# Kernel tuning notes

Hardware: AMD Instinct MI355X
Metric: run time of the kernel (lower is better)

The kernel has to match this reference:

```python
import jax, jax.numpy as jnp
import numpy as np

EPS = 1.0       # epsilon
SIGMA = 1.0     # sigma
MAX_ITER = 10   # max_iter (tol=1e-6 never triggers early stop in 10 iters for random data)


def setup_inputs() -> dict:
    key = jax.random.key(0)
    k1, k2, k3, k4 = jax.random.split(key, 4)
    B, L, K, D = 8, 2048, 2048, 64
    x = jax.random.normal(k1, (B, L, D), dtype=jnp.float32)
    y = jax.random.normal(k2, (B, K, D), dtype=jnp.float32)
    a = jax.random.uniform(k3, (B, L), dtype=jnp.float32) + 1e-3
    b = jax.random.uniform(k4, (B, K), dtype=jnp.float32) + 1e-3
    a = a / jnp.sum(a, axis=1, keepdims=True)
    b = b / jnp.sum(b, axis=1, keepdims=True)
    return {"x": x, "a": a, "y": y, "b": b}


def _make_kernel(u, v):
    # energy_squared, distance_type=2: K = -clamp(||u||^2 + ||v||^2 - 2 u.v, 0) / sigma^2
    outer = jnp.einsum('bld,bkd->blk', u, v)
    nu = jnp.sum(u * u, axis=2)
    nv = jnp.sum(v * v, axis=2)
    dist = jnp.maximum(nu[:, :, None] + nv[:, None, :] - 2.0 * outer, 0.0) / (SIGMA ** 2)
    return -dist


def _extrap(pot, logw, kern):
    # -eps * logsumexp((K + pot[:,None,:]) / eps + logw[:,None,:], axis=2)
    return -EPS * jax.scipy.special.logsumexp(
        (kern + pot[:, None, :]) / EPS + logw[:, None, :], axis=2)


def reference(x, a, y, b):
    sg = jax.lax.stop_gradient
    Kxx = _make_kernel(x, x)
    Kyy = _make_kernel(y, y)
    Kxy = _make_kernel(x, y)
    Kyx = _make_kernel(y, x)
    la = jnp.log(a)
    lb = jnp.log(b)

    # Sinkhorn fixed-point loop runs under no_grad in the original ('loop' surgery)
    sKxx, sKyy, sKxy, sKyx = sg(Kxx), sg(Kyy), sg(Kxy), sg(Kyx)
    sla, slb = sg(la), sg(lb)

    def body(i, state):
        pxx, pyy, pxy, pyx = state
        nxx = _extrap(pxx, sla, sKxx)  # dir 'xx', rev 'xx'
        nyy = _extrap(pyy, slb, sKyy)  # dir 'yy', rev 'yy'
        nxy = _extrap(pyx, slb, sKxy)  # dir 'xy', rev 'yx'
        nyx = _extrap(pxy, sla, sKyx)  # dir 'yx', rev 'xy'
        return ((nxx + pxx) * 0.5, (nyy + pyy) * 0.5,
                (nxy + pxy) * 0.5, (nyx + pyx) * 0.5)

    init = (jnp.zeros_like(la), jnp.zeros_like(lb),
            jnp.zeros_like(la), jnp.zeros_like(lb))
    pxx, pyy, pxy, pyx = jax.lax.fori_loop(0, MAX_ITER, body, init)
    pxx, pyy, pxy, pyx = sg(pxx), sg(pyy), sg(pxy), sg(pyx)

    # Final differentiable extrapolation (rho=None -> potential_transform is identity)
    f = _extrap(pxx, la, Kxx)   # (B, L)
    fe = _extrap(pxy, la, Kyx)  # (B, K)
    g = _extrap(pyy, lb, Kyy)   # (B, K)
    ge = _extrap(pyx, lb, Kxy)  # (B, L)

    diff_r = jnp.where(a == 0, 0.0, ge - f)
    diff_l = jnp.where(b == 0, 0.0, fe - g)
    res = jnp.sum(diff_r * a, axis=1) + jnp.sum(diff_l * b, axis=1)
    return jnp.mean(res)
```

## Files before the change

kernel.cpp:

```cpp
#include <hip/hip_runtime.h>
#include <stdint.h>

#define BATCH 8
#define NPTS  2048
#define DIM   64
#define VECN  (BATCH*NPTS)
#define KH    1024
#define CHUNK 64
#define NCHUNK (KH/CHUNK)

typedef __attribute__((ext_vector_type(8))) short bf16x8;
typedef __attribute__((ext_vector_type(4))) float f32x4;

#define IL2 1.4426950408889634f
#define LN2 0.6931471805599453f

__device__ inline float fexp2(float x) { return __builtin_amdgcn_exp2f(x); }
__device__ inline float flog2(float x) { return __builtin_amdgcn_logf(x); }

__device__ inline void gload_lds16(const void* g, void* l) {
  __builtin_amdgcn_global_load_lds(
      (const __attribute__((address_space(1))) uint32_t*)g,
      (__attribute__((address_space(3))) uint32_t*)l, 16, 0, 0);
}
__device__ inline void gload_lds4(const void* g, void* l) {
  __builtin_amdgcn_global_load_lds(
      (const __attribute__((address_space(1))) uint32_t*)g,
      (__attribute__((address_space(3))) uint32_t*)l, 4, 0, 0);
}

static constexpr size_t XB_OFF   = 0;
static constexpr size_t YB_OFF   = (size_t)VECN * DIM * 2;
static constexpr size_t NX2_OFF  = YB_OFF * 2;
static constexpr size_t NY2_OFF  = NX2_OFF + (size_t)VECN * 4;
static constexpr size_t LA2_OFF  = NY2_OFF + (size_t)VECN * 4;
static constexpr size_t LB2_OFF  = LA2_OFF + (size_t)VECN * 4;
static constexpr size_t POT_OFF  = LB2_OFF + (size_t)VECN * 4;
static constexpr size_t NW_OFF   = POT_OFF + (size_t)4 * VECN * 4;
static constexpr size_t PM_OFF   = NW_OFF + (size_t)4 * VECN * 8;
static constexpr size_t PS_OFF   = PM_OFF + (size_t)8 * VECN * 4;
static constexpr size_t FOUT_OFF = PS_OFF + (size_t)8 * VECN * 4;
static constexpr size_t R_OFF    = FOUT_OFF + (size_t)4 * VECN * 4;

__device__ inline ushort f2bf(float f) {
  uint32_t u = __float_as_uint(f);
  u += 0x7fffu + ((u >> 16) & 1u);
  return (ushort)(u >> 16);
}

__global__ void prep_convert(const float* __restrict__ x, const float* __restrict__ y,
                             ushort* __restrict__ xb, ushort* __restrict__ yb,
                             float* __restrict__ nx2, float* __restrict__ ny2) {
  int wid  = (blockIdx.x * blockDim.x + threadIdx.x) >> 6;
  int lane = threadIdx.x & 63;
  const float* src; ushort* dst; float* nrm; int row;
  if (wid < VECN) { src = x; dst = xb; nrm = nx2; row = wid; }
  else            { src = y; dst = yb; nrm = ny2; row = wid - VECN; }
  float v = src[(size_t)row * DIM + lane];
  dst[(size_t)row * DIM + lane] = f2bf(v);
  float sq = v * v;
  #pragma unroll
  for (int off = 32; off; off >>= 1) sq += __shfl_xor(sq, off);
  if (lane == 0) nrm[row] = sq * IL2;
}

__global__ void prep_vecs(const float* __restrict__ a, const float* __restrict__ b,
                          const float* __restrict__ nx2, const float* __restrict__ ny2,
                          float* __restrict__ la2, float* __restrict__ lb2,
                          float* __restrict__ pot, float2* __restrict__ nw) {
  int i = blockIdx.x * blockDim.x + threadIdx.x;
  float l2a = log2f(a[i]);
  float l2b = log2f(b[i]);
  la2[i] = l2a;
  lb2[i] = l2b;
  float nxv = nx2[i], nyv = ny2[i];
  nw[i]                     = make_float2(nxv, l2a);
  nw[(size_t)VECN + i]      = make_float2(nyv, l2b);
  nw[(size_t)2 * VECN + i]  = make_float2(nyv, l2b);
  nw[(size_t)3 * VECN + i]  = make_float2(nxv, l2a);
  #pragma unroll
  for (int j = 0; j < 4; ++j) pot[(size_t)j * VECN + i] = 0.f;
}

__global__ __launch_bounds__(256, 8)
void extrap_online(const ushort* __restrict__ xb, const ushort* __restrict__ yb,
                   const float* __restrict__ nx2, const float* __restrict__ ny2,
                   const float2* __restrict__ nw,
                   float* __restrict__ pm, float* __restrict__ ps) {
  __shared__ char vlds[2][CHUNK * 128];
  __shared__ char nwlds[2][CHUNK * 8];

  const int rb    = blockIdx.x >> 1;
  const int half  = blockIdx.x & 1;
  const int batch = blockIdx.y;
  const int z     = blockIdx.z;
  const ushort *U, *V; const float *nU2;
  switch (z) {
    case 0:  U = xb; V = xb; nU2 = nx2; break;
    case 1:  U = yb; V = yb; nU2 = ny2; break;
    case 2:  U = xb; V = yb; nU2 = nx2; break;
    default: U = yb; V = xb; nU2 = ny2; break;
  }
  const int lane = threadIdx.x & 63;
  const int w    = threadIdx.x >> 6;
  const int g    = lane >> 4;
  const int c    = lane & 15;
  const int rowbase = rb * 64 + w * 16;

  const ushort* Ub  = U + ((size_t)batch * NPTS + rowbase) * DIM;
  const char*   Vch = (const char*)(V + ((size_t)batch * NPTS + half * KH) * DIM);
  const char*   nwch = (const char*)(nw + (size_t)z * VECN + (size_t)batch * NPTS + half * KH);

  bf16x8 a0 = *(const bf16x8*)(Ub + (size_t)c * DIM + g * 8);
  bf16x8 a1 = *(const bf16x8*)(Ub + (size_t)c * DIM + 32 + g * 8);

  float nxr2[4];
  #pragma unroll
  for (int r = 0; r < 4; ++r) nxr2[r] = nU2[(size_t)batch * NPTS + rowbase + g * 4 + r];

  const size_t lane_voff = ((size_t)(lane >> 3)) * 128
                         + (size_t)((((lane & 7) ^ (lane >> 3)) << 4));

  float m[4], s[4];
  #pragma unroll
  for (int r = 0; r < 4; ++r) { m[r] = -INFINITY; s[r] = 0.f; }

  auto stage = [&](int p, int ck) {
    const char* gbase = Vch + (size_t)ck * CHUNK * 128;
    #pragma unroll
    for (int i = 0; i < 2; ++i) {
      int j = w * 2 + i;
      gload_lds16(gbase + (size_t)j * 1024 + lane_voff, &vlds[p][j * 1024]);
    }
    if (w == 0) {
      const char* gn = nwch + (size_t)ck * CHUNK * 8;
      gload_lds4(gn + lane * 4,       &nwlds[p][0]);
      gload_lds4(gn + 256 + lane * 4, &nwlds[p][256]);
    }
  };

  auto compute = [&](int p) {
    #pragma unroll
    for (int t = 0; t < 2; ++t) {
      const int rr0 = t * 32 + c;
      const int rr1 = rr0 + 16;
      const int x0 = (rr0 & 7) << 4;
      const char* pv0 = &vlds[p][rr0 * 128];
      const char* pv1 = &vlds[p][rr1 * 128];
      bf16x8 b0a = *(const bf16x8*)(pv0 + ((g * 16) ^ x0));
      bf16x8 b0b = *(const bf16x8*)(pv0 + ((64 + g * 16) ^ x0));
      bf16x8 b1a = *(const bf16x8*)(pv1 + ((g * 16) ^ x0));
      bf16x8 b1b = *(const bf16x8*)(pv1 + ((64 + g * 16) ^ x0));
      float2 nw0 = *(const float2*)&nwlds[p][rr0 * 8];
      float2 nw1 = *(const float2*)&nwlds[p][rr1 * 8];

      f32x4 acc0 = {0.f, 0.f, 0.f, 0.f}, acc1 = {0.f, 0.f, 0.f, 0.f};
      acc0 = __builtin_amdgcn_mfma_f32_16x16x32_bf16(a0, b0a, acc0, 0, 0, 0);
      acc0 = __builtin_amdgcn_mfma_f32_16x16x32_bf16(a1, b0b, acc0, 0, 0, 0);
      acc1 = __builtin_amdgcn_mfma_f32_16x16x32_bf16(a0, b1a, acc1, 0, 0, 0);
      acc1 = __builtin_amdgcn_mfma_f32_16x16x32_bf16(a1, b1b, acc1, 0, 0, 0);

      #pragma unroll
      for (int r = 0; r < 4; ++r) {
        float d0 = fmaxf(fmaf(-2.f * IL2, acc0[r], nxr2[r] + nw0.x), 0.f);
        float d1 = fmaxf(fmaf(-2.f * IL2, acc1[r], nxr2[r] + nw1.x), 0.f);
        float t0 = nw0.y - d0;
        float t1 = nw1.y - d1;
        float mn = fmaxf(m[r], fmaxf(t0, t1));
        s[r] = fmaf(s[r], fexp2(m[r] - mn), fexp2(t0 - mn) + fexp2(t1 - mn));
        m[r] = mn;
      }
    }
  };

  stage(0, 0);
  __syncthreads();
  int p = 0;
  for (int ck = 0; ck < NCHUNK; ++ck) {
    if (ck < NCHUNK - 1) stage(p ^ 1, ck + 1);
    compute(p);
    __syncthreads();
    p ^= 1;
  }

  #pragma unroll
  for (int r = 0; r < 4; ++r) {
    #pragma unroll
    for (int off = 1; off < 16; off <<= 1) {
      float mo = __shfl_xor(m[r], off);
      float so = __shfl_xor(s[r], off);
      float mn = fmaxf(m[r], mo);
      s[r] = fmaf(s[r], fexp2(m[r] - mn), so * fexp2(mo - mn));
      m[r] = mn;
    }
  }
  if (c == 0) {
    #pragma unroll
    for (int r = 0; r < 4; ++r) {
      size_t idx = (size_t)(half * 4 + z) * VECN + (size_t)batch * NPTS + rowbase + g * 4 + r;
      pm[idx] = m[r];
      ps[idx] = s[r];
    }
  }
}

__global__ __launch_bounds__(256, 8)
void extrap_fixed(const ushort* __restrict__ xb, const ushort* __restrict__ yb,
                  const float* __restrict__ nx2, const float* __restrict__ ny2,
                  const float2* __restrict__ nw, const float* __restrict__ Rarr,
                  float* __restrict__ pm, float* __restrict__ ps) {
  __shared__ char vlds[2][CHUNK * 128];
  __shared__ char nwlds[2][CHUNK * 8];

  const int rb    = blockIdx.x >> 1;
  const int half  = blockIdx.x & 1;
  const int batch = blockIdx.y;
  const int z     = blockIdx.z;
  const ushort *U, *V; const float *nU2;
  switch (z) {
    case 0:  U = xb; V = xb; nU2 = nx2; break;
    case 1:  U = yb; V = yb; nU2 = ny2; break;
    case 2:  U = xb; V = yb; nU2 = nx2; break;
    default: U = yb; V = xb; nU2 = ny2; break;
  }
  const int lane = threadIdx.x & 63;
  const int w    = threadIdx.x >> 6;
  const int g    = lane >> 4;
  const int c    = lane & 15;
  const int rowbase = rb * 64 + w * 16;

  const ushort* Ub  = U + ((size_t)batch * NPTS + rowbase) * DIM;
  const char*   Vch = (const char*)(V + ((size_t)batch * NPTS + half * KH) * DIM);
  const char*   nwch = (const char*)(nw + (size_t)z * VECN + (size_t)batch * NPTS + half * KH);

  bf16x8 a0 = *(const bf16x8*)(Ub + (size_t)c * DIM + g * 8);
  bf16x8 a1 = *(const bf16x8*)(Ub + (size_t)c * DIM + 32 + g * 8);

  float q[4], Rr[4];
  #pragma unroll
  for (int r = 0; r < 4; ++r) {
    size_t rowi = (size_t)batch * NPTS + rowbase + g * 4 + r;
    Rr[r] = Rarr[(size_t)z * VECN + rowi];
    q[r]  = -(nU2[rowi] + Rr[r]);
  }

  const size_t lane_voff = ((size_t)(lane >> 3)) * 128
                         + (size_t)((((lane & 7) ^ (lane >> 3)) << 4));

  float s[4] = {0.f, 0.f, 0.f, 0.f};

  auto stage = [&](int p, int ck) {
    const char* gbase = Vch + (size_t)ck * CHUNK * 128;
    #pragma unroll
    for (int i = 0; i < 2; ++i) {
      int j = w * 2 + i;
      gload_lds16(gbase + (size_t)j * 1024 + lane_voff, &vlds[p][j * 1024]);
    }
    if (w == 0) {
      const char* gn = nwch + (size_t)ck * CHUNK * 8;
      gload_lds4(gn + lane * 4,       &nwlds[p][0]);
      gload_lds4(gn + 256 + lane * 4, &nwlds[p][256]);
    }
  };

  auto compute = [&](int p) {
    #pragma unroll
    for (int t = 0; t < 2; ++t) {
      const int rr0 = t * 32 + c;
      const int rr1 = rr0 + 16;
      const int x0 = (rr0 & 7) << 4;
      const char* pv0 = &vlds[p][rr0 * 128];
      const char* pv1 = &vlds[p][rr1 * 128];
      bf16x8 b0a = *(const bf16x8*)(pv0 + ((g * 16) ^ x0));
      bf16x8 b0b = *(const bf16x8*)(pv0 + ((64 + g * 16) ^ x0));
      bf16x8 b1a = *(const bf16x8*)(pv1 + ((g * 16) ^ x0));
      bf16x8 b1b = *(const bf16x8*)(pv1 + ((64 + g * 16) ^ x0));
      float2 nw0 = *(const float2*)&nwlds[p][rr0 * 8];
      float2 nw1 = *(const float2*)&nwlds[p][rr1 * 8];
      float ct0 = nw0.y - nw0.x;
      float ct1 = nw1.y - nw1.x;

      f32x4 acc0 = {0.f, 0.f, 0.f, 0.f}, acc1 = {0.f, 0.f, 0.f, 0.f};
      acc0 = __builtin_amdgcn_mfma_f32_16x16x32_bf16(a0, b0a, acc0, 0, 0, 0);
      acc0 = __builtin_amdgcn_mfma_f32_16x16x32_bf16(a1, b0b, acc0, 0, 0, 0);
      acc1 = __builtin_amdgcn_mfma_f32_16x16x32_bf16(a0, b1a, acc1, 0, 0, 0);
      acc1 = __builtin_amdgcn_mfma_f32_16x16x32_bf16(a1, b1b, acc1, 0, 0, 0);

      #pragma unroll
      for (int r = 0; r < 4; ++r) {
        s[r] += fexp2(fmaf(2.f * IL2, acc0[r], ct0 + q[r]));
        s[r] += fexp2(fmaf(2.f * IL2, acc1[r], ct1 + q[r]));
      }
    }
  };

  stage(0, 0);
  __syncthreads();
  int p = 0;
  for (int ck = 0; ck < NCHUNK; ++ck) {
    if (ck < NCHUNK - 1) stage(p ^ 1, ck + 1);
    compute(p);
    __syncthreads();
    p ^= 1;
  }

  #pragma unroll
  for (int r = 0; r < 4; ++r) {
    #pragma unroll
    for (int off = 1; off < 16; off <<= 1) s[r] += __shfl_xor(s[r], off);
  }
  if (c == 0) {
    #pragma unroll
    for (int r = 0; r < 4; ++r) {
      size_t idx = (size_t)(half * 4 + z) * VECN + (size_t)batch * NPTS + rowbase + g * 4 + r;
      pm[idx] = Rr[r];
      ps[idx] = s[r];
    }
  }
}

__global__ void merge_kernel(const float* __restrict__ pm, const float* __restrict__ ps,
                             float* __restrict__ pot,
                             const float* __restrict__ la2, const float* __restrict__ lb2,
                             float2* __restrict__ nw, float* __restrict__ Rarr,
                             float* __restrict__ fouts, int avg) {
  int i = blockIdx.x * blockDim.x + threadIdx.x;
  int z = i >> 14;
  int iin = i & (VECN - 1);
  float m0 = pm[i], m1 = pm[(size_t)4 * VECN + i];
  float s0 = ps[i], s1 = ps[(size_t)4 * VECN + i];
  float mn = fmaxf(m0, m1);
  float s  = fmaf(s0, fexp2(m0 - mn), s1 * fexp2(m1 - mn));
  s = fmaxf(s, 1e-38f);
  float lse = mn + flog2(s);
  float val = -LN2 * lse;
  if (avg) {
    val = 0.5f * (val + pot[i]);
    pot[i] = val;
    Rarr[i] = lse;
    int cjob = z ^ (z >> 1);
    const float* lw2 = (z & 1) ? lb2 : la2;
    nw[(size_t)cjob * VECN + iin].y = fmaf(val, IL2, lw2[iin]);
  } else {
    fouts[i] = val;
  }
}

__global__ void reduce_kernel(const float* __restrict__ fouts,
                              const float* __restrict__ a, const float* __restrict__ b,
                              float* __restrict__ out) {
  const float* f  = fouts;
  const float* g  = fouts + (size_t)VECN;
  const float* ge = fouts + (size_t)2 * VECN;
  const float* fe = fouts + (size_t)3 * VECN;
  int tid = threadIdx.x;
  float acc = 0.f;
  for (int i = tid; i < VECN; i += 1024)
    acc += (ge[i] - f[i]) * a[i] + (fe[i] - g[i]) * b[i];
  #pragma unroll
  for (int off = 32; off; off >>= 1) acc += __shfl_xor(acc, off);
  __shared__ float red[16];
  if ((tid & 63) == 0) red[tid >> 6] = acc;
  __syncthreads();
  if (tid < 64) {
    float v = (tid < 16) ? red[tid] : 0.f;
    #pragma unroll
    for (int off = 8; off; off >>= 1) v += __shfl_xor(v, off);
    if (tid == 0) out[0] = v / (float)BATCH;
  }
}

extern "C" void kernel_launch(void* const* d_in, const int* in_sizes, int n_in,
                              void* d_out, int out_size, void* d_ws, size_t ws_size,
                              hipStream_t stream) {
  const float* x = (const float*)d_in[0];
  const float* a = (const float*)d_in[1];
  const float* y = (const float*)d_in[2];
  const float* b = (const float*)d_in[3];
  char* ws = (char*)d_ws;
  ushort* xb  = (ushort*)(ws + XB_OFF);
  ushort* yb  = (ushort*)(ws + YB_OFF);
  float* nx2  = (float*)(ws + NX2_OFF);
  float* ny2  = (float*)(ws + NY2_OFF);
  float* la2  = (float*)(ws + LA2_OFF);
  float* lb2  = (float*)(ws + LB2_OFF);
  float* pot  = (float*)(ws + POT_OFF);
  float2* nw  = (float2*)(ws + NW_OFF);
  float* pm   = (float*)(ws + PM_OFF);
  float* ps   = (float*)(ws + PS_OFF);
  float* fouts= (float*)(ws + FOUT_OFF);
  float* Rarr = (float*)(ws + R_OFF);

  prep_convert<<<dim3(2 * VECN / 4), 256, 0, stream>>>(x, y, xb, yb, nx2, ny2);
  prep_vecs<<<dim3(VECN / 256), 256, 0, stream>>>(a, b, nx2, ny2, la2, lb2, pot, nw);

  const dim3 eg((NPTS / 64) * 2, BATCH, 4);
  extrap_online<<<eg, 256, 0, stream>>>(xb, yb, nx2, ny2, nw, pm, ps);
  merge_kernel<<<dim3(4 * VECN / 256), 256, 0, stream>>>(
      pm, ps, pot, la2, lb2, nw, Rarr, fouts, 1);
  for (int it = 1; it < 10; ++it) {
    extrap_fixed<<<eg, 256, 0, stream>>>(xb, yb, nx2, ny2, nw, Rarr, pm, ps);
    merge_kernel<<<dim3(4 * VECN / 256), 256, 0, stream>>>(
        pm, ps, pot, la2, lb2, nw, Rarr, fouts, 1);
  }
  extrap_fixed<<<eg, 256, 0, stream>>>(xb, yb, nx2, ny2, nw, Rarr, pm, ps);
  merge_kernel<<<dim3(4 * VECN / 256), 256, 0, stream>>>(
      pm, ps, pot, la2, lb2, nw, Rarr, fouts, 0);

  reduce_kernel<<<1, 1024, 0, stream>>>(fouts, a, b, (float*)d_out);
}
```

Before: 486.3 us.

## Process four 16-row tiles per wave to reuse staged V chunks

Each wave now handles 64 rows (four MFMA row tiles) instead of 16, so each block covers 256 rows and reuses every LDS-staged V chunk and its nw values four times. This cuts global-to-LDS staging traffic and LDS B-operand reads per unit of work by four. In exchange, per-thread register use grows (A fragments, running max/sum, norms), launch bounds drop to 2 blocks per SM, and the grid shrinks from 4096 to 1024 blocks. That lowers occupancy and latency hiding on a device with many compute units.

```diff
diff --git a/kernel.cpp b/kernel.cpp
--- a/kernel.cpp
+++ b/kernel.cpp
@@ -8,6 +8,8 @@
 #define KH    1024
 #define CHUNK 64
 #define NCHUNK (KH/CHUNK)
+#define ROWS_PER_WAVE 64
+#define ROWS_PER_BLOCK 256
 
 typedef __attribute__((ext_vector_type(8))) short bf16x8;
 typedef __attribute__((ext_vector_type(4))) float f32x4;
@@ -82,7 +84,7 @@
   for (int j = 0; j < 4; ++j) pot[(size_t)j * VECN + i] = 0.f;
 }
 
-__global__ __launch_bounds__(256, 8)
+__global__ __launch_bounds__(256, 2)
 void extrap_online(const ushort* __restrict__ xb, const ushort* __restrict__ yb,
                    const float* __restrict__ nx2, const float* __restrict__ ny2,
                    const float2* __restrict__ nw,
@@ -105,25 +107,34 @@
   const int w    = threadIdx.x >> 6;
   const int g    = lane >> 4;
   const int c    = lane & 15;
-  const int rowbase = rb * 64 + w * 16;
+  const int rowbase = rb * ROWS_PER_BLOCK + w * ROWS_PER_WAVE;
 
   const ushort* Ub  = U + ((size_t)batch * NPTS + rowbase) * DIM;
   const char*   Vch = (const char*)(V + ((size_t)batch * NPTS + half * KH) * DIM);
   const char*   nwch = (const char*)(nw + (size_t)z * VECN + (size_t)batch * NPTS + half * KH);
 
-  bf16x8 a0 = *(const bf16x8*)(Ub + (size_t)c * DIM + g * 8);
-  bf16x8 a1 = *(const bf16x8*)(Ub + (size_t)c * DIM + 32 + g * 8);
-
-  float nxr2[4];
-  #pragma unroll
-  for (int r = 0; r < 4; ++r) nxr2[r] = nU2[(size_t)batch * NPTS + rowbase + g * 4 + r];
+  bf16x8 a0[4], a1[4];
+  #pragma unroll
+  for (int rt = 0; rt < 4; ++rt) {
+    a0[rt] = *(const bf16x8*)(Ub + (size_t)(rt * 16 + c) * DIM + g * 8);
+    a1[rt] = *(const bf16x8*)(Ub + (size_t)(rt * 16 + c) * DIM + 32 + g * 8);
+  }
+
+  float nxr2[4][4];
+  #pragma unroll
+  for (int rt = 0; rt < 4; ++rt)
+    #pragma unroll
+    for (int r = 0; r < 4; ++r)
+      nxr2[rt][r] = nU2[(size_t)batch * NPTS + rowbase + rt * 16 + g * 4 + r];
 
   const size_t lane_voff = ((size_t)(lane >> 3)) * 128
                          + (size_t)((((lane & 7) ^ (lane >> 3)) << 4));
 
-  float m[4], s[4];
-  #pragma unroll
-  for (int r = 0; r < 4; ++r) { m[r] = -INFINITY; s[r] = 0.f; }
+  float m[4][4], s[4][4];
+  #pragma unroll
+  for (int rt = 0; rt < 4; ++rt)
+    #pragma unroll
+    for (int r = 0; r < 4; ++r) { m[rt][r] = -INFINITY; s[rt][r] = 0.f; }
 
   auto stage = [&](int p, int ck) {
     const char* gbase = Vch + (size_t)ck * CHUNK * 128;
@@ -154,21 +165,24 @@
       float2 nw0 = *(const float2*)&nwlds[p][rr0 * 8];
       float2 nw1 = *(const float2*)&nwlds[p][rr1 * 8];
 
-      f32x4 acc0 = {0.f, 0.f, 0.f, 0.f}, acc1 = {0.f, 0.f, 0.f, 0.f};
-      acc0 = __builtin_amdgcn_mfma_f32_16x16x32_bf16(a0, b0a, acc0, 0, 0, 0);
-      acc0 = __builtin_amdgcn_mfma_f32_16x16x32_bf16(a1, b0b, acc0, 0, 0, 0);
-      acc1 = __builtin_amdgcn_mfma_f32_16x16x32_bf16(a0, b1a, acc1, 0, 0, 0);
-      acc1 = __builtin_amdgcn_mfma_f32_16x16x32_bf16(a1, b1b, acc1, 0, 0, 0);
-
-      #pragma unroll
-      for (int r = 0; r < 4; ++r) {
-        float d0 = fmaxf(fmaf(-2.f * IL2, acc0[r], nxr2[r] + nw0.x), 0.f);
-        float d1 = fmaxf(fmaf(-2.f * IL2, acc1[r], nxr2[r] + nw1.x), 0.f);
-        float t0 = nw0.y - d0;
-        float t1 = nw1.y - d1;
-        float mn = fmaxf(m[r], fmaxf(t0, t1));
-        s[r] = fmaf(s[r], fexp2(m[r] - mn), fexp2(t0 - mn) + fexp2(t1 - mn));
-        m[r] = mn;
+      #pragma unroll
+      for (int rt = 0; rt < 4; ++rt) {
+        f32x4 acc0 = {0.f, 0.f, 0.f, 0.f}, acc1 = {0.f, 0.f, 0.f, 0.f};
+        acc0 = __builtin_amdgcn_mfma_f32_16x16x32_bf16(a0[rt], b0a, acc0, 0, 0, 0);
+        acc0 = __builtin_amdgcn_mfma_f32_16x16x32_bf16(a1[rt], b0b, acc0, 0, 0, 0);
+        acc1 = __builtin_amdgcn_mfma_f32_16x16x32_bf16(a0[rt], b1a, acc1, 0, 0, 0);
+        acc1 = __builtin_amdgcn_mfma_f32_16x16x32_bf16(a1[rt], b1b, acc1, 0, 0, 0);
+
+        #pragma unroll
+        for (int r = 0; r < 4; ++r) {
+          float d0 = fmaxf(fmaf(-2.f * IL2, acc0[r], nxr2[rt][r] + nw0.x), 0.f);
+          float d1 = fmaxf(fmaf(-2.f * IL2, acc1[r], nxr2[rt][r] + nw1.x), 0.f);
+          float t0 = nw0.y - d0;
+          float t1 = nw1.y - d1;
+          float mn = fmaxf(m[rt][r], fmaxf(t0, t1));
+          s[rt][r] = fmaf(s[rt][r], fexp2(m[rt][r] - mn), fexp2(t0 - mn) + fexp2(t1 - mn));
+          m[rt][r] = mn;
+        }
       }
     }
   };
@@ -184,27 +198,33 @@
   }
 
   #pragma unroll
-  for (int r = 0; r < 4; ++r) {
-    #pragma unroll
-    for (int off = 1; off < 16; off <<= 1) {
-      float mo = __shfl_xor(m[r], off);
-      float so = __shfl_xor(s[r], off);
-      float mn = fmaxf(m[r], mo);
-      s[r] = fmaf(s[r], fexp2(m[r] - mn), so * fexp2(mo - mn));
-      m[r] = mn;
+  for (int rt = 0; rt < 4; ++rt) {
+    #pragma unroll
+    for (int r = 0; r < 4; ++r) {
+      #pragma unroll
+      for (int off = 1; off < 16; off <<= 1) {
+        float mo = __shfl_xor(m[rt][r], off);
+        float so = __shfl_xor(s[rt][r], off);
+        float mn = fmaxf(m[rt][r], mo);
+        s[rt][r] = fmaf(s[rt][r], fexp2(m[rt][r] - mn), so * fexp2(mo - mn));
+        m[rt][r] = mn;
+      }
     }
   }
   if (c == 0) {
     #pragma unroll
-    for (int r = 0; r < 4; ++r) {
-      size_t idx = (size_t)(half * 4 + z) * VECN + (size_t)batch * NPTS + rowbase + g * 4 + r;
-      pm[idx] = m[r];
-      ps[idx] = s[r];
-    }
-  }
-}
-
-__global__ __launch_bounds__(256, 8)
+    for (int rt = 0; rt < 4; ++rt)
+      #pragma unroll
+      for (int r = 0; r < 4; ++r) {
+        size_t idx = (size_t)(half * 4 + z) * VECN + (size_t)batch * NPTS
+                   + rowbase + rt * 16 + g * 4 + r;
+        pm[idx] = m[rt][r];
+        ps[idx] = s[rt][r];
+      }
+  }
+}
+
+__global__ __launch_bounds__(256, 2)
 void extrap_fixed(const ushort* __restrict__ xb, const ushort* __restrict__ yb,
                   const float* __restrict__ nx2, const float* __restrict__ ny2,
                   const float2* __restrict__ nw, const float* __restrict__ Rarr,
@@ -227,27 +247,37 @@
   const int w    = threadIdx.x >> 6;
   const int g    = lane >> 4;
   const int c    = lane & 15;
-  const int rowbase = rb * 64 + w * 16;
+  const int rowbase = rb * ROWS_PER_BLOCK + w * ROWS_PER_WAVE;
 
   const ushort* Ub  = U + ((size_t)batch * NPTS + rowbase) * DIM;
   const char*   Vch = (const char*)(V + ((size_t)batch * NPTS + half * KH) * DIM);
   const char*   nwch = (const char*)(nw + (size_t)z * VECN + (size_t)batch * NPTS + half * KH);
 
-  bf16x8 a0 = *(const bf16x8*)(Ub + (size_t)c * DIM + g * 8);
-  bf16x8 a1 = *(const bf16x8*)(Ub + (size_t)c * DIM + 32 + g * 8);
-
-  float q[4], Rr[4];
-  #pragma unroll
-  for (int r = 0; r < 4; ++r) {
-    size_t rowi = (size_t)batch * NPTS + rowbase + g * 4 + r;
-    Rr[r] = Rarr[(size_t)z * VECN + rowi];
-    q[r]  = -(nU2[rowi] + Rr[r]);
-  }
+  bf16x8 a0[4], a1[4];
+  #pragma unroll
+  for (int rt = 0; rt < 4; ++rt) {
+    a0[rt] = *(const bf16x8*)(Ub + (size_t)(rt * 16 + c) * DIM + g * 8);
+    a1[rt] = *(const bf16x8*)(Ub + (size_t)(rt * 16 + c) * DIM + 32 + g * 8);
+  }
+
+  float q[4][4], Rr[4][4];
+  #pragma unroll
+  for (int rt = 0; rt < 4; ++rt)
+    #pragma unroll
+    for (int r = 0; r < 4; ++r) {
+      size_t rowi = (size_t)batch * NPTS + rowbase + rt * 16 + g * 4 + r;
+      Rr[rt][r] = Rarr[(size_t)z * VECN + rowi];
+      q[rt][r]  = -(nU2[rowi] + Rr[rt][r]);
+    }
 
   const size_t lane_voff = ((size_t)(lane >> 3)) * 128
                          + (size_t)((((lane & 7) ^ (lane >> 3)) << 4));
 
-  float s[4] = {0.f, 0.f, 0.f, 0.f};
+  float s[4][4];
+  #pragma unroll
+  for (int rt = 0; rt < 4; ++rt)
+    #pragma unroll
+    for (int r = 0; r < 4; ++r) s[rt][r] = 0.f;
 
   auto stage = [&](int p, int ck) {
     const char* gbase = Vch + (size_t)ck * CHUNK * 128;
@@ -280,16 +310,19 @@
       float ct0 = nw0.y - nw0.x;
       float ct1 = nw1.y - nw1.x;
 
-      f32x4 acc0 = {0.f, 0.f, 0.f, 0.f}, acc1 = {0.f, 0.f, 0.f, 0.f};
-      acc0 = __builtin_amdgcn_mfma_f32_16x16x32_bf16(a0, b0a, acc0, 0, 0, 0);
-      acc0 = __builtin_amdgcn_mfma_f32_16x16x32_bf16(a1, b0b, acc0, 0, 0, 0);
-      acc1 = __builtin_amdgcn_mfma_f32_16x16x32_bf16(a0, b1a, acc1, 0, 0, 0);
-      acc1 = __builtin_amdgcn_mfma_f32_16x16x32_bf16(a1, b1b, acc1, 0, 0, 0);
-
-      #pragma unroll
-      for (int r = 0; r < 4; ++r) {
-        s[r] += fexp2(fmaf(2.f * IL2, acc0[r], ct0 + q[r]));
-        s[r] += fexp2(fmaf(2.f * IL2, acc1[r], ct1 + q[r]));
+      #pragma unroll
+      for (int rt = 0; rt < 4; ++rt) {
+        f32x4 acc0 = {0.f, 0.f, 0.f, 0.f}, acc1 = {0.f, 0.f, 0.f, 0.f};
+        acc0 = __builtin_amdgcn_mfma_f32_16x16x32_bf16(a0[rt], b0a, acc0, 0, 0, 0);
+        acc0 = __builtin_amdgcn_mfma_f32_16x16x32_bf16(a1[rt], b0b, acc0, 0, 0, 0);
+        acc1 = __builtin_amdgcn_mfma_f32_16x16x32_bf16(a0[rt], b1a, acc1, 0, 0, 0);
+        acc1 = __builtin_amdgcn_mfma_f32_16x16x32_bf16(a1[rt], b1b, acc1, 0, 0, 0);
+
+        #pragma unroll
+        for (int r = 0; r < 4; ++r) {
+          s[rt][r] += fexp2(fmaf(2.f * IL2, acc0[r], ct0 + q[rt][r]));
+          s[rt][r] += fexp2(fmaf(2.f * IL2, acc1[r], ct1 + q[rt][r]));
+        }
       }
     }
   };
@@ -305,17 +338,23 @@
   }
 
   #pragma unroll
-  for (int r = 0; r < 4; ++r) {
-    #pragma unroll
-    for (int off = 1; off < 16; off <<= 1) s[r] += __shfl_xor(s[r], off);
+  for (int rt = 0; rt < 4; ++rt) {
+    #pragma unroll
+    for (int r = 0; r < 4; ++r) {
+      #pragma unroll
+      for (int off = 1; off < 16; off <<= 1) s[rt][r] += __shfl_xor(s[rt][r], off);
+    }
   }
   if (c == 0) {
     #pragma unroll
-    for (int r = 0; r < 4; ++r) {
-      size_t idx = (size_t)(half * 4 + z) * VECN + (size_t)batch * NPTS + rowbase + g * 4 + r;
-      pm[idx] = Rr[r];
-      ps[idx] = s[r];
-    }
+    for (int rt = 0; rt < 4; ++rt)
+      #pragma unroll
+      for (int r = 0; r < 4; ++r) {
+        size_t idx = (size_t)(half * 4 + z) * VECN + (size_t)batch * NPTS
+                   + rowbase + rt * 16 + g * 4 + r;
+        pm[idx] = Rr[rt][r];
+        ps[idx] = s[rt][r];
+      }
   }
 }
 
@@ -394,7 +433,7 @@
   prep_convert<<<dim3(2 * VECN / 4), 256, 0, stream>>>(x, y, xb, yb, nx2, ny2);
   prep_vecs<<<dim3(VECN / 256), 256, 0, stream>>>(a, b, nx2, ny2, la2, lb2, pot, nw);
 
-  const dim3 eg((NPTS / 64) * 2, BATCH, 4);
+  const dim3 eg((NPTS / ROWS_PER_BLOCK) * 2, BATCH, 4);
   extrap_online<<<eg, 256, 0, stream>>>(xb, yb, nx2, ny2, nw, pm, ps);
   merge_kernel<<<dim3(4 * VECN / 256), 256, 0, stream>>>(
       pm, ps, pot, la2, lb2, nw, Rarr, fouts, 1);
```

Result: no change. 493.4 us (+1.5%).

## Drop split-K halves and fuse the merge step into the extrapolation kernels

Applied to the files above, without the earlier changes.

Each extrapolation block now covers the full 2048-column reduction instead of half, so the partial max/sum buffers and the separate merge kernel go away. The log-sum-exp finalisation, potential averaging and weight update happen in the extrapolation epilogue. The weight buffer is double-buffered so blocks can write new weights while others still read the old ones. This removes eleven kernel launches and the partial-result traffic. In exchange the grid is halved, so each block runs twice as long and fewer waves are resident per CU to hide latency.

```diff
diff --git a/kernel.cpp b/kernel.cpp
--- a/kernel.cpp
+++ b/kernel.cpp
@@ -5,9 +5,8 @@
 #define NPTS  2048
 #define DIM   64
 #define VECN  (BATCH*NPTS)
-#define KH    1024
 #define CHUNK 64
-#define NCHUNK (KH/CHUNK)
+#define NCHUNK (NPTS/CHUNK)
 
 typedef __attribute__((ext_vector_type(8))) short bf16x8;
 typedef __attribute__((ext_vector_type(4))) float f32x4;
@@ -36,10 +35,9 @@
 static constexpr size_t LA2_OFF  = NY2_OFF + (size_t)VECN * 4;
 static constexpr size_t LB2_OFF  = LA2_OFF + (size_t)VECN * 4;
 static constexpr size_t POT_OFF  = LB2_OFF + (size_t)VECN * 4;
-static constexpr size_t NW_OFF   = POT_OFF + (size_t)4 * VECN * 4;
-static constexpr size_t PM_OFF   = NW_OFF + (size_t)4 * VECN * 8;
-static constexpr size_t PS_OFF   = PM_OFF + (size_t)8 * VECN * 4;
-static constexpr size_t FOUT_OFF = PS_OFF + (size_t)8 * VECN * 4;
+static constexpr size_t NW0_OFF  = POT_OFF + (size_t)4 * VECN * 4;
+static constexpr size_t NW1_OFF  = NW0_OFF + (size_t)4 * VECN * 8;
+static constexpr size_t FOUT_OFF = NW1_OFF + (size_t)4 * VECN * 8;
 static constexpr size_t R_OFF    = FOUT_OFF + (size_t)4 * VECN * 4;
 
 __device__ inline ushort f2bf(float f) {
@@ -67,17 +65,19 @@
 __global__ void prep_vecs(const float* __restrict__ a, const float* __restrict__ b,
                           const float* __restrict__ nx2, const float* __restrict__ ny2,
                           float* __restrict__ la2, float* __restrict__ lb2,
-                          float* __restrict__ pot, float2* __restrict__ nw) {
+                          float* __restrict__ pot,
+                          float2* __restrict__ nw0, float2* __restrict__ nw1) {
   int i = blockIdx.x * blockDim.x + threadIdx.x;
   float l2a = log2f(a[i]);
   float l2b = log2f(b[i]);
   la2[i] = l2a;
   lb2[i] = l2b;
   float nxv = nx2[i], nyv = ny2[i];
-  nw[i]                     = make_float2(nxv, l2a);
-  nw[(size_t)VECN + i]      = make_float2(nyv, l2b);
-  nw[(size_t)2 * VECN + i]  = make_float2(nyv, l2b);
-  nw[(size_t)3 * VECN + i]  = make_float2(nxv, l2a);
+  float2 vx = make_float2(nxv, l2a), vy = make_float2(nyv, l2b);
+  nw0[i]                    = vx;  nw1[i]                    = vx;
+  nw0[(size_t)VECN + i]     = vy;  nw1[(size_t)VECN + i]     = vy;
+  nw0[(size_t)2*VECN + i]   = vy;  nw1[(size_t)2*VECN + i]   = vy;
+  nw0[(size_t)3*VECN + i]   = vx;  nw1[(size_t)3*VECN + i]   = vx;
   #pragma unroll
   for (int j = 0; j < 4; ++j) pot[(size_t)j * VECN + i] = 0.f;
 }
@@ -85,13 +85,14 @@
 __global__ __launch_bounds__(256, 8)
 void extrap_online(const ushort* __restrict__ xb, const ushort* __restrict__ yb,
                    const float* __restrict__ nx2, const float* __restrict__ ny2,
-                   const float2* __restrict__ nw,
-                   float* __restrict__ pm, float* __restrict__ ps) {
+                   const float2* __restrict__ nwin, float2* __restrict__ nwout,
+                   const float* __restrict__ la2, const float* __restrict__ lb2,
+                   float* __restrict__ pot, float* __restrict__ Rarr,
+                   float* __restrict__ fouts, int avg) {
   __shared__ char vlds[2][CHUNK * 128];
   __shared__ char nwlds[2][CHUNK * 8];
 
-  const int rb    = blockIdx.x >> 1;
-  const int half  = blockIdx.x & 1;
+  const int rb    = blockIdx.x;
   const int batch = blockIdx.y;
   const int z     = blockIdx.z;
   const ushort *U, *V; const float *nU2;
@@ -108,8 +109,8 @@
   const int rowbase = rb * 64 + w * 16;
 
   const ushort* Ub  = U + ((size_t)batch * NPTS + rowbase) * DIM;
-  const char*   Vch = (const char*)(V + ((size_t)batch * NPTS + half * KH) * DIM);
-  const char*   nwch = (const char*)(nw + (size_t)z * VECN + (size_t)batch * NPTS + half * KH);
+  const char*   Vch = (const char*)(V + (size_t)batch * NPTS * DIM);
+  const char*   nwch = (const char*)(nwin + (size_t)z * VECN + (size_t)batch * NPTS);
 
   bf16x8 a0 = *(const bf16x8*)(Ub + (size_t)c * DIM + g * 8);
   bf16x8 a1 = *(const bf16x8*)(Ub + (size_t)c * DIM + 32 + g * 8);
@@ -195,11 +196,22 @@
     }
   }
   if (c == 0) {
+    const int cjob = z ^ (z >> 1);
+    const float* lw2 = (z & 1) ? lb2 : la2;
     #pragma unroll
     for (int r = 0; r < 4; ++r) {
-      size_t idx = (size_t)(half * 4 + z) * VECN + (size_t)batch * NPTS + rowbase + g * 4 + r;
-      pm[idx] = m[r];
-      ps[idx] = s[r];
+      int rowi = batch * NPTS + rowbase + g * 4 + r;
+      size_t pi = (size_t)z * VECN + rowi;
+      float lse = m[r] + flog2(fmaxf(s[r], 1e-38f));
+      float val = -LN2 * lse;
+      if (avg) {
+        val = 0.5f * (val + pot[pi]);
+        pot[pi] = val;
+        Rarr[pi] = lse;
+        nwout[(size_t)cjob * VECN + rowi].y = fmaf(val, IL2, lw2[rowi]);
+      } else {
+        fouts[pi] = val;
+      }
     }
   }
 }
@@ -207,13 +219,14 @@
 __global__ __launch_bounds__(256, 8)
 void extrap_fixed(const ushort* __restrict__ xb, const ushort* __restrict__ yb,
                   const float* __restrict__ nx2, const float* __restrict__ ny2,
-                  const float2* __restrict__ nw, const float* __restrict__ Rarr,
-                  float* __restrict__ pm, float* __restrict__ ps) {
+                  const float2* __restrict__ nwin, float2* __restrict__ nwout,
+                  const float* __restrict__ la2, const float* __restrict__ lb2,
+                  float* __restrict__ pot, float* __restrict__ Rarr,
+                  float* __restrict__ fouts, int avg) {
   __shared__ char vlds[2][CHUNK * 128];
   __shared__ char nwlds[2][CHUNK * 8];
 
-  const int rb    = blockIdx.x >> 1;
-  const int half  = blockIdx.x & 1;
+  const int rb    = blockIdx.x;
   const int batch = blockIdx.y;
   const int z     = blockIdx.z;
   const ushort *U, *V; const float *nU2;
@@ -230,8 +243,8 @@
   const int rowbase = rb * 64 + w * 16;
 
   const ushort* Ub  = U + ((size_t)batch * NPTS + rowbase) * DIM;
-  const char*   Vch = (const char*)(V + ((size_t)batch * NPTS + half * KH) * DIM);
-  const char*   nwch = (const char*)(nw + (size_t)z * VECN + (size_t)batch * NPTS + half * KH);
+  const char*   Vch = (const char*)(V + (size_t)batch * NPTS * DIM);
+  const char*   nwch = (const char*)(nwin + (size_t)z * VECN + (size_t)batch * NPTS);
 
   bf16x8 a0 = *(const bf16x8*)(Ub + (size_t)c * DIM + g * 8);
   bf16x8 a1 = *(const bf16x8*)(Ub + (size_t)c * DIM + 32 + g * 8);
@@ -310,39 +323,23 @@
     for (int off = 1; off < 16; off <<= 1) s[r] += __shfl_xor(s[r], off);
   }
   if (c == 0) {
+    const int cjob = z ^ (z >> 1);
+    const float* lw2 = (z & 1) ? lb2 : la2;
     #pragma unroll
     for (int r = 0; r < 4; ++r) {
-      size_t idx = (size_t)(half * 4 + z) * VECN + (size_t)batch * NPTS + rowbase + g * 4 + r;
-      pm[idx] = Rr[r];
-      ps[idx] = s[r];
-    }
-  }
-}
-
-__global__ void merge_kernel(const float* __restrict__ pm, const float* __restrict__ ps,
-                             float* __restrict__ pot,
-                             const float* __restrict__ la2, const float* __restrict__ lb2,
-                             float2* __restrict__ nw, float* __restrict__ Rarr,
-                             float* __restrict__ fouts, int avg) {
-  int i = blockIdx.x * blockDim.x + threadIdx.x;
-  int z = i >> 14;
-  int iin = i & (VECN - 1);
-  float m0 = pm[i], m1 = pm[(size_t)4 * VECN + i];
-  float s0 = ps[i], s1 = ps[(size_t)4 * VECN + i];
-  float mn = fmaxf(m0, m1);
-  float s  = fmaf(s0, fexp2(m0 - mn), s1 * fexp2(m1 - mn));
-  s = fmaxf(s, 1e-38f);
-  float lse = mn + flog2(s);
-  float val = -LN2 * lse;
-  if (avg) {
-    val = 0.5f * (val + pot[i]);
-    pot[i] = val;
-    Rarr[i] = lse;
-    int cjob = z ^ (z >> 1);
-    const float* lw2 = (z & 1) ? lb2 : la2;
-    nw[(size_t)cjob * VECN + iin].y = fmaf(val, IL2, lw2[iin]);
-  } else {
-    fouts[i] = val;
+      int rowi = batch * NPTS + rowbase + g * 4 + r;
+      size_t pi = (size_t)z * VECN + rowi;
+      float lse = Rr[r] + flog2(fmaxf(s[r], 1e-38f));
+      float val = -LN2 * lse;
+      if (avg) {
+        val = 0.5f * (val + pot[pi]);
+        pot[pi] = val;
+        Rarr[pi] = lse;
+        nwout[(size_t)cjob * VECN + rowi].y = fmaf(val, IL2, lw2[rowi]);
+      } else {
+        fouts[pi] = val;
+      }
+    }
   }
 }
 
@@ -385,27 +382,26 @@
   float* la2  = (float*)(ws + LA2_OFF);
   float* lb2  = (float*)(ws + LB2_OFF);
   float* pot  = (float*)(ws + POT_OFF);
-  float2* nw  = (float2*)(ws + NW_OFF);
-  float* pm   = (float*)(ws + PM_OFF);
-  float* ps   = (float*)(ws + PS_OFF);
+  float2* nw0 = (float2*)(ws + NW0_OFF);
+  float2* nw1 = (float2*)(ws + NW1_OFF);
   float* fouts= (float*)(ws + FOUT_OFF);
   float* Rarr = (float*)(ws + R_OFF);
 
   prep_convert<<<dim3(2 * VECN / 4), 256, 0, stream>>>(x, y, xb, yb, nx2, ny2);
-  prep_vecs<<<dim3(VECN / 256), 256, 0, stream>>>(a, b, nx2, ny2, la2, lb2, pot, nw);
-
-  const dim3 eg((NPTS / 64) * 2, BATCH, 4);
-  extrap_online<<<eg, 256, 0, stream>>>(xb, yb, nx2, ny2, nw, pm, ps);
-  merge_kernel<<<dim3(4 * VECN / 256), 256, 0, stream>>>(
-      pm, ps, pot, la2, lb2, nw, Rarr, fouts, 1);
+  prep_vecs<<<dim3(VECN / 256), 256, 0, stream>>>(a, b, nx2, ny2, la2, lb2, pot, nw0, nw1);
+
+  const dim3 eg(NPTS / 64, BATCH, 4);
+  float2* bufs[2] = {nw0, nw1};
+  extrap_online<<<eg, 256, 0, stream>>>(xb, yb, nx2, ny2, bufs[0], bufs[1],
+                                        la2, lb2, pot, Rarr, fouts, 1);
   for (int it = 1; it < 10; ++it) {
-    extrap_fixed<<<eg, 256, 0, stream>>>(xb, yb, nx2, ny2, nw, Rarr, pm, ps);
-    merge_kernel<<<dim3(4 * VECN / 256), 256, 0, stream>>>(
-        pm, ps, pot, la2, lb2, nw, Rarr, fouts, 1);
-  }
-  extrap_fixed<<<eg, 256, 0, stream>>>(xb, yb, nx2, ny2, nw, Rarr, pm, ps);
-  merge_kernel<<<dim3(4 * VECN / 256), 256, 0, stream>>>(
-      pm, ps, pot, la2, lb2, nw, Rarr, fouts, 0);
+    extrap_fixed<<<eg, 256, 0, stream>>>(xb, yb, nx2, ny2,
+                                         bufs[it & 1], bufs[(it & 1) ^ 1],
+                                         la2, lb2, pot, Rarr, fouts, 1);
+  }
+  extrap_fixed<<<eg, 256, 0, stream>>>(xb, yb, nx2, ny2,
+                                       bufs[10 & 1], bufs[(10 & 1) ^ 1],
+                                       la2, lb2, pot, Rarr, fouts, 0);
 
   reduce_kernel<<<1, 1024, 0, stream>>>(fouts, a, b, (float*)d_out);
 }
```

New measurement: 505.6 us. 1.04x slower.
